# Kernel tuning notes

Hardware: AMD Instinct MI355X
Metric: run time of the kernel (lower is better)

The kernel has to match this reference:

```python
import jax, jax.numpy as jnp
import numpy as np

T_SEG = 8      # n_segment
KSZ = 3        # LAM temporal kernel size
PAD = 1        # LAM temporal padding
BN_EPS = 1e-5


def setup_inputs() -> dict:
    key = jax.random.key(0)
    ks = jax.random.split(key, 12)
    n, t, c, h, w = 8, T_SEG, 256, 56, 56
    return {
        "x": jax.random.normal(ks[0], (n * t, c, h, w), jnp.float32),
        "net_w": jax.random.normal(ks[1], (c, c, 3, 3), jnp.float32) * 0.02,
        "net_b": jax.random.normal(ks[2], (c,), jnp.float32) * 0.02,
        "lam_w": jax.random.normal(ks[3], (c, c), jnp.float32) * 0.02,
        "lam_b": jax.random.normal(ks[4], (c,), jnp.float32) * 0.02,
        "mlp_w1": jax.random.normal(ks[5], (2 * t, t), jnp.float32) * 0.3,
        "bn_gamma": jax.random.uniform(ks[6], (2 * t,), jnp.float32, 0.5, 1.5),
        "bn_beta": jax.random.normal(ks[7], (2 * t,), jnp.float32) * 0.1,
        "bn_mean": jax.random.normal(ks[8], (2 * t,), jnp.float32) * 0.1,
        "bn_var": jax.random.uniform(ks[9], (2 * t,), jnp.float32, 0.5, 1.5),
        "mlp_w2": jax.random.normal(ks[10], (KSZ, 2 * t), jnp.float32) * 0.3,
        "me_w": jax.random.normal(ks[11], (3,), jnp.float32) * 0.3,
    }


def reference(x, net_w, net_b, lam_w, lam_b, mlp_w1, bn_gamma, bn_beta,
              bn_mean, bn_var, mlp_w2, me_w):
    t = T_SEG
    nt, c, h, w = x.shape
    n = nt // t

    # --- wrapped net: Conv2d 3x3, pad 1 ---
    out = jax.lax.conv_general_dilated(
        x, net_w, window_strides=(1, 1), padding="SAME",
        dimension_numbers=("NCHW", "OIHW", "NCHW"))
    out = out + net_b[None, :, None, None]

    # --- LAM ---
    new_x = out.reshape(n, t, c, h, w).transpose(0, 2, 1, 3, 4)  # (n,c,t,h,w)
    x_g = new_x.mean(axis=(2, 3, 4))                   # global pool -> (n,c)
    x_g = x_g @ lam_w.T + lam_b                        # Conv1d k=1 == matmul
    new_x = new_x + x_g[:, :, None, None, None]

    pooled = new_x.mean(axis=(3, 4)).reshape(n * c, t)  # per-(n,c) temporal sig
    hdn = pooled @ mlp_w1.T                              # (n*c, 2t), no bias
    hdn = (hdn - bn_mean) * (bn_gamma / jnp.sqrt(bn_var + BN_EPS)) + bn_beta
    hdn = jax.nn.relu(hdn)
    wgt = jax.nn.softmax(hdn @ mlp_w2.T, axis=-1).reshape(n, c, KSZ)

    # grouped conv2d (groups=n*c) == per-(n,c) depthwise temporal conv
    xpad = jnp.pad(new_x, ((0, 0), (0, 0), (PAD, PAD), (0, 0), (0, 0)))
    lam_out = sum(wgt[:, :, k, None, None, None] * xpad[:, :, k:k + t]
                  for k in range(KSZ))                  # (n,c,t,h,w)
    lam_out = lam_out.transpose(0, 2, 1, 3, 4).reshape(nt, c, h, w)

    # --- ME ---
    xv = lam_out.reshape(n, t, c, h, w)
    diff = xv[:, 1:] - xv[:, :-1]                       # frame differences
    diff = jnp.pad(diff, ((0, 0), (0, 1), (0, 0), (0, 0), (0, 0)))
    diff = diff.reshape(nt, c, h, w)
    y = diff.mean(axis=(2, 3))                          # (nt, c)
    ypad = jnp.pad(y, ((0, 0), (1, 1)))                 # conv1d over channel dim
    yc = sum(me_w[k] * ypad[:, k:k + c] for k in range(3))
    gate = jax.nn.sigmoid(yc)[:, :, None, None]

    return gate * lam_out
```

## Files before the change

### kernel.cpp

```cpp
#include <hip/hip_runtime.h>
#include <hip/hip_bf16.h>
#include <stdint.h>

#define AS1 __attribute__((address_space(1)))
#define AS3 __attribute__((address_space(3)))

typedef __attribute__((ext_vector_type(8))) short short8v;
typedef __attribute__((ext_vector_type(4))) float float4v;

#define NT 64
#define CCH 256
#define HH 56
#define WW 56
#define HWSZ 3136
#define HP 58
#define WP 58

#define OFF_XT   0ull
#define SZ_XT    110231552ull
#define OFF_WPK  (OFF_XT + SZ_XT)
#define SZ_WPK   1179648ull
#define OFF_CS   (OFF_WPK + SZ_WPK)
#define SZ_CS    65536ull
#define OFF_XG2  (OFF_CS + SZ_CS)
#define SZ_XG2   8192ull
#define OFF_WGT  (OFF_XG2 + SZ_XG2)
#define SZ_WGT   24576ull
#define OFF_M    (OFF_WGT + SZ_WGT)
#define SZ_M     65536ull
#define OFF_GATE (OFF_M + SZ_M)
#define SZ_GATE  65536ull

__device__ __forceinline__ unsigned short f2bf(float f) {
    unsigned int u = __float_as_uint(f);
    unsigned int r = (u + 0x7fffu + ((u >> 16) & 1u)) >> 16;
    return (unsigned short)r;
}

__device__ __forceinline__ void gload16(const unsigned short* g, unsigned short* l) {
    __builtin_amdgcn_global_load_lds((const AS1 void*)g, (AS3 void*)l, 16, 0, 0);
}

__global__ __launch_bounds__(256) void k0_transpose(const float* __restrict__ x,
                                                    unsigned short* __restrict__ xt) {
    int b = blockIdx.x;
    int cb = b & 3;
    int h  = (b >> 2) % 56;
    int nt = b / (4 * 56);
    int c0 = cb * 64;
    int tid = threadIdx.x;

    __shared__ float xs[64 * 57];

    const float* src = x + ((size_t)nt * CCH + c0) * HWSZ + h * WW;
    for (int li = tid; li < 896; li += 256) {
        int row = li / 14, f4 = li % 14;
        float4v v = *(const float4v*)(src + (size_t)row * HWSZ + f4 * 4);
        float* d = &xs[row * 57 + f4 * 4];
        d[0] = v.x; d[1] = v.y; d[2] = v.z; d[3] = v.w;
    }
    __syncthreads();

    unsigned short* dst = xt + (((size_t)nt * HP + (h + 1)) * WP) * CCH + c0;
    for (int job = tid; job < 464; job += 256) {
        int ww = job >> 3, cg = job & 7;
        short8v v;
        if (ww == 0 || ww == 57) {
            v = (short8v){0,0,0,0,0,0,0,0};
        } else {
            #pragma unroll
            for (int jj = 0; jj < 8; ++jj)
                v[jj] = (short)f2bf(xs[(cg * 8 + jj) * 57 + (ww - 1)]);
        }
        *(short8v*)(dst + ww * CCH + cg * 8) = v;
    }
    if (h == 0) {
        unsigned short* d0  = xt + ((size_t)nt * HP + 0)  * WP * CCH + c0;
        unsigned short* d57 = xt + ((size_t)nt * HP + 57) * WP * CCH + c0;
        short8v z = (short8v){0,0,0,0,0,0,0,0};
        for (int job = tid; job < 464; job += 256) {
            int ww = job >> 3, cg = job & 7;
            *(short8v*)(d0  + ww * CCH + cg * 8) = z;
            *(short8v*)(d57 + ww * CCH + cg * 8) = z;
        }
    }
}

__global__ __launch_bounds__(256) void kw_pack(const float* __restrict__ nw,
                                               unsigned short* __restrict__ wpk) {
    int idx = blockIdx.x * 256 + threadIdx.x;
    int rs = idx >> 16;
    int k  = (idx >> 8) & 255;
    int c  = idx & 255;
    wpk[idx] = f2bf(nw[(k * 256 + c) * 9 + rs]);
}


#define STGALL(bi_, tA_, tB_) do { \
    gload16(wpk + (tA_) + aoffg0, &lds[(bi_) * 8192 + ldsa0]); \
    gload16(wpk + (tA_) + aoffg1, &lds[(bi_) * 8192 + ldsa1]); \
    gload16(xt  + (tB_) + boffg,  &lds[24576 + (bi_) * 4096 + ldsb]); \
} while (0)

#define LDAF(mi) (*(const short8v*)&lds[abase + (wm * 64 + (mi) * 16 + r16) * 32 + pA * 8])
#define LDBF(j)  (*(const short8v*)&lds[bbase + (wp * 64 + (j) * 16 + r16) * 32 + pA * 8])

#define BARSYNC do { \
    __builtin_amdgcn_s_barrier(); \
    __builtin_amdgcn_sched_barrier(0); \
} while (0)

__global__ __launch_bounds__(512, 4) void conv_mfma(const unsigned short* __restrict__ xt,
                                                    const unsigned short* __restrict__ wpk,
                                                    const float* __restrict__ net_b,
                                                    float* __restrict__ out,
                                                    float* __restrict__ chansum) {
    __shared__ unsigned short lds[36864];

    const int tid  = threadIdx.x;
    const int lane = tid & 63;
    const int wid  = tid >> 6;
    const int wm   = wid >> 1;
    const int wp   = wid & 1;
    const int r16  = lane & 15;
    const int hi   = lane >> 4;
    const int pA   = (hi + (r16 >> 1)) & 3;

    const int pblk = (blockIdx.x & 7) * 196 + (blockIdx.x >> 3);
    const int p0 = pblk * 128;

    const int cgs = ((tid & 3) - (tid >> 3)) & 3;
    const int aoffg0 = (tid >> 2) * 256 + cgs * 8;
    const int aoffg1 = aoffg0 + 32768;
    const int ldsa0  = tid * 8;
    const int ldsa1  = ldsa0 + 4096;
    const int ldsb   = tid * 8;
    long boffg;
    {
        int r = tid >> 2;
        int p = p0 + r;
        int nt = p / HWSZ, hw = p - nt * HWSZ;
        int hh = hw / WW,  w  = hw - hh * WW;
        boffg = ((long)(nt * HP + hh) * WP + w) * 256 + cgs * 8;
    }

    float4v acc[4][4];
    #pragma unroll
    for (int i = 0; i < 4; ++i)
        #pragma unroll
        for (int j = 0; j < 4; ++j) acc[i][j] = (float4v){0.f, 0.f, 0.f, 0.f};

    STGALL(0, 0, 0);
    {
        const int tA1 = 32, tB1 = 32;
        STGALL(1, tA1, tB1);
    }

    int cur = 0;
    for (int kt = 0; kt < 72; ++kt) {
        const int abase = cur * 8192;
        const int bbase = 24576 + cur * 4096;

        if (kt < 70) {
            const int ktn = kt + 2;
            int nb2 = cur + 2; if (nb2 >= 3) nb2 -= 3;
            const int rsn = ktn >> 3, con = (ktn & 7) * 32;
            const int tAn = rsn * 65536 + con;
            const int tBn = ((rsn / 3) * WP + (rsn - (rsn / 3) * 3)) * 256 + con;
            STGALL(nb2, tAn, tBn);
            asm volatile("s_waitcnt vmcnt(6)" ::: "memory");
        } else if (kt == 70) {
            asm volatile("s_waitcnt vmcnt(3)" ::: "memory");
        } else {
            asm volatile("s_waitcnt vmcnt(0)" ::: "memory");
        }
        BARSYNC;

        short8v afrag[4], bfrag[4];
        #pragma unroll
        for (int mi = 0; mi < 4; ++mi) afrag[mi] = LDAF(mi);
        #pragma unroll
        for (int j = 0; j < 4; ++j) bfrag[j] = LDBF(j);

        asm volatile("s_waitcnt lgkmcnt(0)" ::: "memory");
        __builtin_amdgcn_sched_barrier(0);
        __builtin_amdgcn_s_setprio(1);
        #pragma unroll
        for (int j = 0; j < 4; ++j)
            #pragma unroll
            for (int mi = 0; mi < 4; ++mi)
                acc[mi][j] = __builtin_amdgcn_mfma_f32_16x16x32_bf16(afrag[mi], bfrag[j], acc[mi][j], 0, 0, 0);
        __builtin_amdgcn_s_setprio(0);
        BARSYNC;

        ++cur; if (cur >= 3) cur = 0;
    }

    const int pw = p0 + wp * 64;
    const int ntw = pw / HWSZ;
    const int hwb = pw - ntw * HWSZ;
    #pragma unroll
    for (int mi = 0; mi < 4; ++mi) {
        #pragma unroll
        for (int r = 0; r < 4; ++r) {
            const int m = wm * 64 + mi * 16 + hi * 4 + r;
            const float bias = net_b[m];
            float csum = 0.f;
            float* orow = out + ((size_t)ntw * CCH + m) * HWSZ + hwb;
            #pragma unroll
            for (int j = 0; j < 4; ++j) {
                float v = acc[mi][j][r] + bias;
                orow[j * 16 + r16] = v;
                csum += v;
            }
            csum += __shfl_xor(csum, 1);
            csum += __shfl_xor(csum, 2);
            csum += __shfl_xor(csum, 4);
            csum += __shfl_xor(csum, 8);
            if (r16 == 0) atomicAdd(&chansum[ntw * CCH + m], csum);
        }
    }
}

__global__ __launch_bounds__(256) void k2_xg(const float* __restrict__ chansum,
                                             const float* __restrict__ lam_w,
                                             const float* __restrict__ lam_b,
                                             float* __restrict__ xg2) {
    int n = blockIdx.x, c = threadIdx.x;
    __shared__ float xs[256];
    float s = 0.f;
    #pragma unroll
    for (int t = 0; t < 8; ++t) s += chansum[(n * 8 + t) * CCH + c];
    xs[c] = s * (1.0f / (3136.f * 8.f));
    __syncthreads();
    float d = lam_b[c];
    const float* row = lam_w + c * 256;
    for (int cc = 0; cc < 256; ++cc) d += row[cc] * xs[cc];
    xg2[n * 256 + c] = d;
}

__global__ __launch_bounds__(256) void k3_wgt(const float* __restrict__ chansum,
                                              const float* __restrict__ xg2,
                                              const float* __restrict__ w1,
                                              const float* __restrict__ bg,
                                              const float* __restrict__ bb,
                                              const float* __restrict__ bm,
                                              const float* __restrict__ bv,
                                              const float* __restrict__ w2,
                                              float* __restrict__ wgt,
                                              float* __restrict__ mbuf) {
    int idx = blockIdx.x * 256 + threadIdx.x;
    int n = idx >> 8, c = idx & 255;
    float xg = xg2[idx];
    float p[8];
    #pragma unroll
    for (int t = 0; t < 8; ++t)
        p[t] = chansum[(n * 8 + t) * CCH + c] * (1.0f / 3136.f) + xg;
    float hd[16];
    #pragma unroll
    for (int j = 0; j < 16; ++j) {
        float s = 0.f;
        #pragma unroll
        for (int t = 0; t < 8; ++t) s += p[t] * w1[j * 8 + t];
        s = (s - bm[j]) * (bg[j] * rsqrtf(bv[j] + 1e-5f)) + bb[j];
        hd[j] = fmaxf(s, 0.f);
    }
    float lg[3];
    #pragma unroll
    for (int k = 0; k < 3; ++k) {
        float s = 0.f;
        #pragma unroll
        for (int j = 0; j < 16; ++j) s += hd[j] * w2[k * 16 + j];
        lg[k] = s;
    }
    float mx = fmaxf(fmaxf(lg[0], lg[1]), lg[2]);
    float e0 = expf(lg[0] - mx), e1 = expf(lg[1] - mx), e2 = expf(lg[2] - mx);
    float inv = 1.f / (e0 + e1 + e2);
    float wk[3] = {e0 * inv, e1 * inv, e2 * inv};
    #pragma unroll
    for (int k = 0; k < 3; ++k) wgt[idx * 3 + k] = wk[k];
    #pragma unroll
    for (int t = 0; t < 8; ++t) {
        float s = 0.f;
        #pragma unroll
        for (int k = 0; k < 3; ++k) {
            int tt = t + k - 1;
            if (tt >= 0 && tt < 8) s += wk[k] * p[tt];
        }
        mbuf[idx * 8 + t] = s;
    }
}

__global__ __launch_bounds__(256) void k4_gate(const float* __restrict__ mbuf,
                                               const float* __restrict__ me_w,
                                               float* __restrict__ gate) {
    int b = blockIdx.x;
    int n = b >> 3, t = b & 7;
    int c = threadIdx.x;
    __shared__ float y[256];
    float yv = 0.f;
    if (t < 7) yv = mbuf[(n * 256 + c) * 8 + t + 1] - mbuf[(n * 256 + c) * 8 + t];
    y[c] = yv;
    __syncthreads();
    float yc = me_w[1] * yv;
    if (c > 0)   yc += me_w[0] * y[c - 1];
    if (c < 255) yc += me_w[2] * y[c + 1];
    gate[b * 256 + c] = 1.f / (1.f + expf(-yc));
}

__global__ __launch_bounds__(256) void k5_final(float* __restrict__ out,
                                                const float* __restrict__ wgt,
                                                const float* __restrict__ xg2,
                                                const float* __restrict__ gate) {
    int tid = blockIdx.x * 256 + threadIdx.x;
    int hw4 = tid % 784;
    int nc = tid / 784;
    int n = nc >> 8, c = nc & 255;
    float w0 = wgt[nc * 3 + 0], w1 = wgt[nc * 3 + 1], w2 = wgt[nc * 3 + 2];
    float xg = xg2[nc];
    const size_t tstride = (size_t)CCH * HWSZ;
    size_t base = ((size_t)(n * 8) * CCH + c) * HWSZ + hw4 * 4;

    float4v o[8];
    #pragma unroll
    for (int t = 0; t < 8; ++t) o[t] = *(const float4v*)(out + base + t * tstride);

    #pragma unroll
    for (int t = 0; t < 8; ++t) {
        float g = gate[(n * 8 + t) * CCH + c];
        float4v lam;
        #pragma unroll
        for (int q = 0; q < 4; ++q) {
            float v = w1 * (o[t][q] + xg);
            if (t > 0) v += w0 * (o[t - 1][q] + xg);
            if (t < 7) v += w2 * (o[t + 1][q] + xg);
            lam[q] = g * v;
        }
        *(float4v*)(out + base + t * tstride) = lam;
    }
}

extern "C" void kernel_launch(void* const* d_in, const int* in_sizes, int n_in,
                              void* d_out, int out_size, void* d_ws, size_t ws_size,
                              hipStream_t stream) {
    const float* x      = (const float*)d_in[0];
    const float* net_w  = (const float*)d_in[1];
    const float* net_b  = (const float*)d_in[2];
    const float* lam_w  = (const float*)d_in[3];
    const float* lam_b  = (const float*)d_in[4];
    const float* mlp_w1 = (const float*)d_in[5];
    const float* bn_g   = (const float*)d_in[6];
    const float* bn_b   = (const float*)d_in[7];
    const float* bn_m   = (const float*)d_in[8];
    const float* bn_v   = (const float*)d_in[9];
    const float* mlp_w2 = (const float*)d_in[10];
    const float* me_w   = (const float*)d_in[11];
    float* out = (float*)d_out;

    char* ws = (char*)d_ws;
    unsigned short* xt  = (unsigned short*)(ws + OFF_XT);
    unsigned short* wpk = (unsigned short*)(ws + OFF_WPK);
    float* chansum = (float*)(ws + OFF_CS);
    float* xg2     = (float*)(ws + OFF_XG2);
    float* wgt     = (float*)(ws + OFF_WGT);
    float* mbuf    = (float*)(ws + OFF_M);
    float* gate    = (float*)(ws + OFF_GATE);

    hipMemsetAsync(chansum, 0, SZ_CS, stream);
    kw_pack<<<2304, 256, 0, stream>>>(net_w, wpk);
    k0_transpose<<<64 * 56 * 4, 256, 0, stream>>>(x, xt);
    conv_mfma<<<1568, 512, 0, stream>>>(xt, wpk, net_b, out, chansum);
    k2_xg<<<8, 256, 0, stream>>>(chansum, lam_w, lam_b, xg2);
    k3_wgt<<<8, 256, 0, stream>>>(chansum, xg2, mlp_w1, bn_g, bn_b, bn_m, bn_v, mlp_w2, wgt, mbuf);
    k4_gate<<<64, 256, 0, stream>>>(mbuf, me_w, gate);
    k5_final<<<6272, 256, 0, stream>>>(out, wgt, xg2, gate);
}
```

Measured before the change: 433.3 us.

## Halve conv block to 4 waves, each computing a 128x64 output tile

Reduces the conv block from 512 to 256 threads while keeping the same 256x128 block tile, so each wave now computes 128 channels by 64 pixels (8x4 MFMA tiles) instead of 64x64. Each thread issues twice as many global-to-LDS loads per stage, and the wait counts are adjusted to match. Per-wave register reuse of B fragments doubles and fewer LDS fragment reads are needed per MFMA, at the cost of more accumulator registers and lower occupancy (launch bounds 256,2).

```diff
diff --git a/kernel.cpp b/kernel.cpp
--- a/kernel.cpp
+++ b/kernel.cpp
@@ -99,10 +99,13 @@
 #define STGALL(bi_, tA_, tB_) do { \
     gload16(wpk + (tA_) + aoffg0, &lds[(bi_) * 8192 + ldsa0]); \
     gload16(wpk + (tA_) + aoffg1, &lds[(bi_) * 8192 + ldsa1]); \
-    gload16(xt  + (tB_) + boffg,  &lds[24576 + (bi_) * 4096 + ldsb]); \
+    gload16(wpk + (tA_) + aoffg2, &lds[(bi_) * 8192 + ldsa2]); \
+    gload16(wpk + (tA_) + aoffg3, &lds[(bi_) * 8192 + ldsa3]); \
+    gload16(xt  + (tB_) + boffg0, &lds[24576 + (bi_) * 4096 + ldsb0]); \
+    gload16(xt  + (tB_) + boffg1, &lds[24576 + (bi_) * 4096 + ldsb1]); \
 } while (0)
 
-#define LDAF(mi) (*(const short8v*)&lds[abase + (wm * 64 + (mi) * 16 + r16) * 32 + pA * 8])
+#define LDAF(mi) (*(const short8v*)&lds[abase + (wm * 128 + (mi) * 16 + r16) * 32 + pA * 8])
 #define LDBF(j)  (*(const short8v*)&lds[bbase + (wp * 64 + (j) * 16 + r16) * 32 + pA * 8])
 
 #define BARSYNC do { \
@@ -110,7 +113,7 @@
     __builtin_amdgcn_sched_barrier(0); \
 } while (0)
 
-__global__ __launch_bounds__(512, 4) void conv_mfma(const unsigned short* __restrict__ xt,
+__global__ __launch_bounds__(256, 2) void conv_mfma(const unsigned short* __restrict__ xt,
                                                     const unsigned short* __restrict__ wpk,
                                                     const float* __restrict__ net_b,
                                                     float* __restrict__ out,
@@ -129,32 +132,42 @@
     const int pblk = (blockIdx.x & 7) * 196 + (blockIdx.x >> 3);
     const int p0 = pblk * 128;
 
-    const int cgs = ((tid & 3) - (tid >> 3)) & 3;
-    const int aoffg0 = (tid >> 2) * 256 + cgs * 8;
-    const int aoffg1 = aoffg0 + 32768;
-    const int ldsa0  = tid * 8;
-    const int ldsa1  = ldsa0 + 4096;
-    const int ldsb   = tid * 8;
-    long boffg;
+    int aoffg0, aoffg1, aoffg2, aoffg3;
+    const int ldsa0 = tid * 8,        ldsa1 = (tid + 256) * 8;
+    const int ldsa2 = (tid + 512) * 8, ldsa3 = (tid + 768) * 8;
+    const int ldsb0 = tid * 8,        ldsb1 = (tid + 256) * 8;
+    long boffg0, boffg1;
     {
-        int r = tid >> 2;
-        int p = p0 + r;
-        int nt = p / HWSZ, hw = p - nt * HWSZ;
-        int hh = hw / WW,  w  = hw - hh * WW;
-        boffg = ((long)(nt * HP + hh) * WP + w) * 256 + cgs * 8;
-    }
-
-    float4v acc[4][4];
-    #pragma unroll
-    for (int i = 0; i < 4; ++i)
+        #pragma unroll
+        for (int i = 0; i < 4; ++i) {
+            int ch = tid + 256 * i;
+            int r = ch >> 2;
+            int cg = ((ch & 3) - (r >> 1)) & 3;
+            int off = r * 256 + cg * 8;
+            if (i == 0) aoffg0 = off; else if (i == 1) aoffg1 = off;
+            else if (i == 2) aoffg2 = off; else aoffg3 = off;
+        }
+        #pragma unroll
+        for (int i = 0; i < 2; ++i) {
+            int ch = tid + 256 * i;
+            int r = ch >> 2;
+            int cg = ((ch & 3) - (r >> 1)) & 3;
+            int p = p0 + r;
+            int nt = p / HWSZ, hw = p - nt * HWSZ;
+            int hh = hw / WW,  w  = hw - hh * WW;
+            long off = ((long)(nt * HP + hh) * WP + w) * 256 + cg * 8;
+            if (i == 0) boffg0 = off; else boffg1 = off;
+        }
+    }
+
+    float4v acc[8][4];
+    #pragma unroll
+    for (int i = 0; i < 8; ++i)
         #pragma unroll
         for (int j = 0; j < 4; ++j) acc[i][j] = (float4v){0.f, 0.f, 0.f, 0.f};
 
     STGALL(0, 0, 0);
-    {
-        const int tA1 = 32, tB1 = 32;
-        STGALL(1, tA1, tB1);
-    }
+    STGALL(1, 32, 32);
 
     int cur = 0;
     for (int kt = 0; kt < 72; ++kt) {
@@ -168,17 +181,17 @@
             const int tAn = rsn * 65536 + con;
             const int tBn = ((rsn / 3) * WP + (rsn - (rsn / 3) * 3)) * 256 + con;
             STGALL(nb2, tAn, tBn);
+            asm volatile("s_waitcnt vmcnt(12)" ::: "memory");
+        } else if (kt == 70) {
             asm volatile("s_waitcnt vmcnt(6)" ::: "memory");
-        } else if (kt == 70) {
-            asm volatile("s_waitcnt vmcnt(3)" ::: "memory");
         } else {
             asm volatile("s_waitcnt vmcnt(0)" ::: "memory");
         }
         BARSYNC;
 
-        short8v afrag[4], bfrag[4];
-        #pragma unroll
-        for (int mi = 0; mi < 4; ++mi) afrag[mi] = LDAF(mi);
+        short8v afrag[8], bfrag[4];
+        #pragma unroll
+        for (int mi = 0; mi < 8; ++mi) afrag[mi] = LDAF(mi);
         #pragma unroll
         for (int j = 0; j < 4; ++j) bfrag[j] = LDBF(j);
 
@@ -188,7 +201,7 @@
         #pragma unroll
         for (int j = 0; j < 4; ++j)
             #pragma unroll
-            for (int mi = 0; mi < 4; ++mi)
+            for (int mi = 0; mi < 8; ++mi)
                 acc[mi][j] = __builtin_amdgcn_mfma_f32_16x16x32_bf16(afrag[mi], bfrag[j], acc[mi][j], 0, 0, 0);
         __builtin_amdgcn_s_setprio(0);
         BARSYNC;
@@ -200,10 +213,10 @@
     const int ntw = pw / HWSZ;
     const int hwb = pw - ntw * HWSZ;
     #pragma unroll
-    for (int mi = 0; mi < 4; ++mi) {
+    for (int mi = 0; mi < 8; ++mi) {
         #pragma unroll
         for (int r = 0; r < 4; ++r) {
-            const int m = wm * 64 + mi * 16 + hi * 4 + r;
+            const int m = wm * 128 + mi * 16 + hi * 4 + r;
             const float bias = net_b[m];
             float csum = 0.f;
             float* orow = out + ((size_t)ntw * CCH + m) * HWSZ + hwb;
@@ -369,7 +382,7 @@
     hipMemsetAsync(chansum, 0, SZ_CS, stream);
     kw_pack<<<2304, 256, 0, stream>>>(net_w, wpk);
     k0_transpose<<<64 * 56 * 4, 256, 0, stream>>>(x, xt);
-    conv_mfma<<<1568, 512, 0, stream>>>(xt, wpk, net_b, out, chansum);
+    conv_mfma<<<1568, 256, 0, stream>>>(xt, wpk, net_b, out, chansum);
     k2_xg<<<8, 256, 0, stream>>>(chansum, lam_w, lam_b, xg2);
     k3_wgt<<<8, 256, 0, stream>>>(chansum, xg2, mlp_w1, bn_g, bn_b, bn_m, bn_v, mlp_w2, wgt, mbuf);
     k4_gate<<<64, 256, 0, stream>>>(mbuf, me_w, gate);
```

After: 443.0 us. +2.2%, slower.
